# Performance work log

Hardware: AMD Instinct MI355X
Metric: run time of the kernel (lower is better)

## Reference

```python
import jax, jax.numpy as jnp
import numpy as np

TS = 0.01  # Euler step size (module's `ts`)

N_X, N_U, N_FEAT = 32, 16, 512
BATCH, SEQ_LEN = 512, 2048


def setup_inputs() -> dict:
    key = jax.random.key(0)
    k0, k1, k2, k3 = jax.random.split(key, 4)
    x0_batch = jax.random.normal(k0, (BATCH, 1, N_X), dtype=jnp.float32)
    u_batch = jax.random.normal(k1, (BATCH, SEQ_LEN, N_U), dtype=jnp.float32)
    # 2-layer MLP state-space model: Linear(n_x+n_u, n_feat) -> Tanh -> Linear(n_feat, n_x)
    fan1 = N_X + N_U
    W1 = jax.random.normal(k2, (fan1, N_FEAT), dtype=jnp.float32) / np.sqrt(fan1).astype(np.float32)
    b1 = jnp.zeros((N_FEAT,), dtype=jnp.float32)
    W2 = jax.random.normal(k3, (N_FEAT, N_X), dtype=jnp.float32) / np.sqrt(N_FEAT).astype(np.float32)
    b2 = jnp.zeros((N_X,), dtype=jnp.float32)
    return {"x0_batch": x0_batch, "u_batch": u_batch, "W1": W1, "b1": b1, "W2": W2, "b2": b2}


def reference(x0_batch, u_batch, W1, b1, W2, b2):
    # x0_batch: (B, 1, n_x); u_batch: (B, T, n_u) -> out: (B, T, n_x)
    x0 = x0_batch[:, 0, :]                       # (B, n_x)
    u_t = jnp.swapaxes(u_batch, 0, 1)            # (T, B, n_u) for scan over time

    def step(x, u):
        h = jnp.tanh(jnp.concatenate([x, u], axis=-1) @ W1 + b1)  # (B, n_feat)
        dx = h @ W2 + b2                                           # (B, n_x)
        x_next = x + TS * dx
        return x_next, x_next

    _, xs = jax.lax.scan(step, x0, u_t)          # xs: (T, B, n_x)
    return jnp.swapaxes(xs, 0, 1)                # (B, T, n_x)
```

## Files before the change

### kernel.cpp

```cpp
#include <hip/hip_runtime.h>

typedef float v2f __attribute__((ext_vector_type(2)));
typedef unsigned uv2 __attribute__((ext_vector_type(2)));

constexpr int NX = 32, NU = 16, NF = 512;
constexpr int SEQ = 2048;
constexpr int NT = 256;
constexpr float SC  = 2.88539008177792681f;
constexpr float TSC = 0.01f;

template<int CTRL>
__device__ __forceinline__ float dpp_mov(float v) {
    return __int_as_float(__builtin_amdgcn_update_dpp(0, __float_as_int(v), CTRL, 0xF, 0xF, true));
}
__device__ __forceinline__ float sum16(float v) {
    uv2 r = __builtin_amdgcn_permlane16_swap(__float_as_uint(v), __float_as_uint(v), false, false);
    return __uint_as_float(r.x) + __uint_as_float(r.y);
}
__device__ __forceinline__ float sum32(float v) {
    uv2 r = __builtin_amdgcn_permlane32_swap(__float_as_uint(v), __float_as_uint(v), false, false);
    return __uint_as_float(r.x) + __uint_as_float(r.y);
}

__device__ __forceinline__ float tanh4(float y) {
    const float e = __builtin_amdgcn_exp2f(y);
    const float r = __builtin_amdgcn_rcpf(e + 1.f);
    return fmaf(-2.f, r, 1.f);
}

__device__ __forceinline__ void bar_lds() {
    asm volatile("s_waitcnt lgkmcnt(0)" ::: "memory");
    __builtin_amdgcn_sched_barrier(0);
    __builtin_amdgcn_s_barrier();
    __builtin_amdgcn_sched_barrier(0);
    asm volatile("" ::: "memory");
}

__global__ __launch_bounds__(NT)
__attribute__((amdgpu_waves_per_eu(2, 2)))
void fes_kernel(const float* __restrict__ x0, const float* __restrict__ ug,
                const float* __restrict__ W1, const float* __restrict__ b1,
                const float* __restrict__ W2, const float* __restrict__ b2,
                float* __restrict__ out)
{
    __shared__ __align__(16) float part[2][NX][12];

    const int tid = threadIdx.x, row = blockIdx.x;
    const int l = tid & 63, w = tid >> 6;

    const int pi = ((l & 1) << 4) | (((l >> 1) & 1) << 3) | (((l >> 3) & 1) << 2)
                 | (((l >> 4) & 1) << 1) | ((l >> 5) & 1);
    const int slot = 2 * w + ((l >> 2) & 1);
    const bool store_lane = (w == 0) && ((l & 4) == 0);

    const int f0 = 2 * tid, f1 = f0 + 1;

    float w1A[32], w1B[32];
#pragma unroll
    for (int k = 0; k < 32; ++k) {
        w1A[k] = SC * W1[k * NF + f0];
        w1B[k] = SC * W1[k * NF + f1];
    }
    v2f wuA[8], wuB[8];
#pragma unroll
    for (int p = 0; p < 8; ++p) {
        const int k = NX + 2 * p;
        wuA[p] = v2f{SC * W1[k * NF + f0], SC * W1[(k + 1) * NF + f0]};
        wuB[p] = v2f{SC * W1[k * NF + f1], SC * W1[(k + 1) * NF + f1]};
    }
    const float b1A = SC * b1[f0], b1B = SC * b1[f1];

    v2f wcA[16], wcB[16];
#pragma unroll
    for (int m = 0; m < 16; ++m) {
        wcA[m] = v2f{TSC * W2[f0 * NX + ((2 * m) ^ pi)], TSC * W2[f0 * NX + ((2 * m + 1) ^ pi)]};
        wcB[m] = v2f{TSC * W2[f1 * NX + ((2 * m) ^ pi)], TSC * W2[f1 * NX + ((2 * m + 1) ^ pi)]};
    }
    const float bb = TSC * b2[pi];
    float xr = x0[row * NX + pi];

    float xu[32];
#pragma unroll
    for (int k = 0; k < 32; ++k) xu[k] = x0[row * NX + k];

    const float* ug_row  = ug  + (size_t)row * SEQ * NU;
    float*       out_row = out + (size_t)row * SEQ * NX;

    float4 u0 = *(const float4*)(ug_row + 0);
    float4 u1 = *(const float4*)(ug_row + 4);
    float4 u2 = *(const float4*)(ug_row + 8);
    float4 u3 = *(const float4*)(ug_row + 12);

#pragma unroll 1
    for (int t = 0; t < SEQ; ++t) {
        float aA0 = b1A, aA1 = 0.f, aA2 = 0.f, aA3 = 0.f;
        float aB0 = b1B, aB1 = 0.f, aB2 = 0.f, aB3 = 0.f;
#pragma unroll
        for (int k = 0; k < 32; k += 4) {
            aA0 = fmaf(w1A[k],     xu[k],     aA0);
            aA1 = fmaf(w1A[k + 1], xu[k + 1], aA1);
            aA2 = fmaf(w1A[k + 2], xu[k + 2], aA2);
            aA3 = fmaf(w1A[k + 3], xu[k + 3], aA3);
            aB0 = fmaf(w1B[k],     xu[k],     aB0);
            aB1 = fmaf(w1B[k + 1], xu[k + 1], aB1);
            aB2 = fmaf(w1B[k + 2], xu[k + 2], aB2);
            aB3 = fmaf(w1B[k + 3], xu[k + 3], aB3);
        }
        v2f uA = {0.f, 0.f}, uB = {0.f, 0.f};
#define UPAIR(uv, p)                                                        \
        { const v2f lo = {uv.x, uv.y}, hi = {uv.z, uv.w};                   \
          uA += wuA[p] * lo;  uA += wuA[p + 1] * hi;                        \
          uB += wuB[p] * lo;  uB += wuB[p + 1] * hi; }
        UPAIR(u0, 0) UPAIR(u1, 2) UPAIR(u2, 4) UPAIR(u3, 6)
#undef UPAIR
        {
            const int tn = (t + 1 < SEQ) ? t + 1 : SEQ - 1;
            const float* un = ug_row + (size_t)tn * NU;
            u0 = *(const float4*)(un + 0);
            u1 = *(const float4*)(un + 4);
            u2 = *(const float4*)(un + 8);
            u3 = *(const float4*)(un + 12);
        }
        const float h0 = tanh4(((aA0 + aA1) + (aA2 + aA3)) + (uA.x + uA.y));
        const float h1 = tanh4(((aB0 + aB1) + (aB2 + aB3)) + (uB.x + uB.y));

        const v2f h0v = {h0, h0}, h1v = {h1, h1};
        v2f q[16];
#pragma unroll
        for (int m = 0; m < 16; ++m)
            q[m] = h0v * wcA[m] + h1v * wcB[m];

#pragma unroll
        for (int m = 0; m < 8; ++m) {
            q[m].x += dpp_mov<0xB1>(q[m + 8].x);
            q[m].y += dpp_mov<0xB1>(q[m + 8].y);
        }
#pragma unroll
        for (int m = 0; m < 4; ++m) {
            q[m].x += dpp_mov<0x4E>(q[m + 4].x);
            q[m].y += dpp_mov<0x4E>(q[m + 4].y);
        }
#pragma unroll
        for (int m = 0; m < 2; ++m) {
            q[m].x += dpp_mov<0x128>(q[m + 2].x);
            q[m].y += dpp_mov<0x128>(q[m + 2].y);
        }
        const float S0 = q[0].x + (sum16(q[1].x) - q[1].x);
        const float S1 = q[0].y + (sum16(q[1].y) - q[1].y);
        const float S  = S0 + (sum32(S1) - S1);

        part[t & 1][pi][slot] = S;
        bar_lds();
        const float4 pa = *(const float4*)&part[t & 1][pi][0];
        const float4 pb4 = *(const float4*)&part[t & 1][pi][4];
        const float dx = (((pa.x + pa.y) + (pa.z + pa.w))
                        + ((pb4.x + pb4.y) + (pb4.z + pb4.w))) + bb;
        const float xn = xr + dx;
        xr = xn;
        if (store_lane) out_row[(size_t)t * NX + pi] = xn;

#pragma unroll
        for (int k = 0; k < 32; ++k) {
            const int L = ((k >> 4) & 1) | (((k >> 3) & 1) << 1) | (((k >> 2) & 1) << 3)
                        | (((k >> 1) & 1) << 4) | ((k & 1) << 5);
            xu[k] = __int_as_float(__builtin_amdgcn_readlane(__float_as_int(xn), L));
        }
    }
}

extern "C" void kernel_launch(void* const* d_in, const int* in_sizes, int n_in,
                              void* d_out, int out_size, void* d_ws, size_t ws_size,
                              hipStream_t stream) {
    const float* x0 = (const float*)d_in[0];
    const float* ug = (const float*)d_in[1];
    const float* W1 = (const float*)d_in[2];
    const float* b1 = (const float*)d_in[3];
    const float* W2 = (const float*)d_in[4];
    const float* b2 = (const float*)d_in[5];
    float* out = (float*)d_out;

    fes_kernel<<<dim3(512), dim3(NT), 0, stream>>>(x0, ug, W1, b1, W2, b2, out);
}
```

Before: 1.979 ms.

## Use 512 threads per block with one hidden feature per thread

Doubles the block size to 512 threads so each thread owns a single hidden feature instead of two. This halves per-thread FMA work and register use per step, and the occupancy hint rises to 4 waves per EU. In exchange the cross-wave LDS reduction grows from 8 to 16 partials per output, with a barrier across 8 waves each step. More waves per block also means more barrier overhead on the serial recurrence.

```diff
diff --git a/kernel.cpp b/kernel.cpp
--- a/kernel.cpp
+++ b/kernel.cpp
@@ -5,7 +5,7 @@
 
 constexpr int NX = 32, NU = 16, NF = 512;
 constexpr int SEQ = 2048;
-constexpr int NT = 256;
+constexpr int NT = 512;
 constexpr float SC  = 2.88539008177792681f;
 constexpr float TSC = 0.01f;
 
@@ -37,13 +37,13 @@
 }
 
 __global__ __launch_bounds__(NT)
-__attribute__((amdgpu_waves_per_eu(2, 2)))
+__attribute__((amdgpu_waves_per_eu(4, 4)))
 void fes_kernel(const float* __restrict__ x0, const float* __restrict__ ug,
                 const float* __restrict__ W1, const float* __restrict__ b1,
                 const float* __restrict__ W2, const float* __restrict__ b2,
                 float* __restrict__ out)
 {
-    __shared__ __align__(16) float part[2][NX][12];
+    __shared__ __align__(16) float part[2][NX][20];
 
     const int tid = threadIdx.x, row = blockIdx.x;
     const int l = tid & 63, w = tid >> 6;
@@ -53,29 +53,24 @@
     const int slot = 2 * w + ((l >> 2) & 1);
     const bool store_lane = (w == 0) && ((l & 4) == 0);
 
-    const int f0 = 2 * tid, f1 = f0 + 1;
+    const int f0 = tid;
 
-    float w1A[32], w1B[32];
+    float w1x[32];
 #pragma unroll
-    for (int k = 0; k < 32; ++k) {
-        w1A[k] = SC * W1[k * NF + f0];
-        w1B[k] = SC * W1[k * NF + f1];
-    }
-    v2f wuA[8], wuB[8];
+    for (int k = 0; k < 32; ++k) w1x[k] = SC * W1[k * NF + f0];
+    v2f wu[8];
 #pragma unroll
     for (int p = 0; p < 8; ++p) {
         const int k = NX + 2 * p;
-        wuA[p] = v2f{SC * W1[k * NF + f0], SC * W1[(k + 1) * NF + f0]};
-        wuB[p] = v2f{SC * W1[k * NF + f1], SC * W1[(k + 1) * NF + f1]};
+        wu[p] = v2f{SC * W1[k * NF + f0], SC * W1[(k + 1) * NF + f0]};
     }
-    const float b1A = SC * b1[f0], b1B = SC * b1[f1];
+    const float b1r = SC * b1[f0];
 
-    v2f wcA[16], wcB[16];
+    v2f wc[16];
 #pragma unroll
-    for (int m = 0; m < 16; ++m) {
-        wcA[m] = v2f{TSC * W2[f0 * NX + ((2 * m) ^ pi)], TSC * W2[f0 * NX + ((2 * m + 1) ^ pi)]};
-        wcB[m] = v2f{TSC * W2[f1 * NX + ((2 * m) ^ pi)], TSC * W2[f1 * NX + ((2 * m + 1) ^ pi)]};
-    }
+    for (int m = 0; m < 16; ++m)
+        wc[m] = v2f{TSC * W2[f0 * NX + ((2 * m) ^ pi)],
+                    TSC * W2[f0 * NX + ((2 * m + 1) ^ pi)]};
     const float bb = TSC * b2[pi];
     float xr = x0[row * NX + pi];
 
@@ -93,24 +88,18 @@
 
 #pragma unroll 1
     for (int t = 0; t < SEQ; ++t) {
-        float aA0 = b1A, aA1 = 0.f, aA2 = 0.f, aA3 = 0.f;
-        float aB0 = b1B, aB1 = 0.f, aB2 = 0.f, aB3 = 0.f;
+        float a0 = b1r, a1 = 0.f, a2 = 0.f, a3 = 0.f;
 #pragma unroll
         for (int k = 0; k < 32; k += 4) {
-            aA0 = fmaf(w1A[k],     xu[k],     aA0);
-            aA1 = fmaf(w1A[k + 1], xu[k + 1], aA1);
-            aA2 = fmaf(w1A[k + 2], xu[k + 2], aA2);
-            aA3 = fmaf(w1A[k + 3], xu[k + 3], aA3);
-            aB0 = fmaf(w1B[k],     xu[k],     aB0);
-            aB1 = fmaf(w1B[k + 1], xu[k + 1], aB1);
-            aB2 = fmaf(w1B[k + 2], xu[k + 2], aB2);
-            aB3 = fmaf(w1B[k + 3], xu[k + 3], aB3);
+            a0 = fmaf(w1x[k],     xu[k],     a0);
+            a1 = fmaf(w1x[k + 1], xu[k + 1], a1);
+            a2 = fmaf(w1x[k + 2], xu[k + 2], a2);
+            a3 = fmaf(w1x[k + 3], xu[k + 3], a3);
         }
-        v2f uA = {0.f, 0.f}, uB = {0.f, 0.f};
+        v2f ua = {0.f, 0.f};
 #define UPAIR(uv, p)                                                        \
         { const v2f lo = {uv.x, uv.y}, hi = {uv.z, uv.w};                   \
-          uA += wuA[p] * lo;  uA += wuA[p + 1] * hi;                        \
-          uB += wuB[p] * lo;  uB += wuB[p + 1] * hi; }
+          ua += wu[p] * lo;  ua += wu[p + 1] * hi; }
         UPAIR(u0, 0) UPAIR(u1, 2) UPAIR(u2, 4) UPAIR(u3, 6)
 #undef UPAIR
         {
@@ -121,14 +110,12 @@
             u2 = *(const float4*)(un + 8);
             u3 = *(const float4*)(un + 12);
         }
-        const float h0 = tanh4(((aA0 + aA1) + (aA2 + aA3)) + (uA.x + uA.y));
-        const float h1 = tanh4(((aB0 + aB1) + (aB2 + aB3)) + (uB.x + uB.y));
+        const float h = tanh4(((a0 + a1) + (a2 + a3)) + (ua.x + ua.y));
 
-        const v2f h0v = {h0, h0}, h1v = {h1, h1};
+        const v2f hv = {h, h};
         v2f q[16];
 #pragma unroll
-        for (int m = 0; m < 16; ++m)
-            q[m] = h0v * wcA[m] + h1v * wcB[m];
+        for (int m = 0; m < 16; ++m) q[m] = hv * wc[m];
 
 #pragma unroll
         for (int m = 0; m < 8; ++m) {
@@ -152,9 +139,13 @@
         part[t & 1][pi][slot] = S;
         bar_lds();
         const float4 pa = *(const float4*)&part[t & 1][pi][0];
-        const float4 pb4 = *(const float4*)&part[t & 1][pi][4];
-        const float dx = (((pa.x + pa.y) + (pa.z + pa.w))
-                        + ((pb4.x + pb4.y) + (pb4.z + pb4.w))) + bb;
+        const float4 pb = *(const float4*)&part[t & 1][pi][4];
+        const float4 pc = *(const float4*)&part[t & 1][pi][8];
+        const float4 pd = *(const float4*)&part[t & 1][pi][12];
+        const float dx = ((((pa.x + pa.y) + (pa.z + pa.w))
+                         + ((pb.x + pb.y) + (pb.z + pb.w)))
+                        + (((pc.x + pc.y) + (pc.z + pc.w))
+                         + ((pd.x + pd.y) + (pd.z + pd.w)))) + bb;
         const float xn = xr + dx;
         xr = xn;
         if (store_lane) out_row[(size_t)t * NX + pi] = xn;
```

Measured after the change: 2.517 ms. 1.27x slower.
